# Performance work log

Hardware: AMD Instinct MI355X
Metric: run time of the kernel (lower is better)

The kernel has to match this reference:

```python
import jax, jax.numpy as jnp
import numpy as np
import math

B, NQ, HID = 1, 512, 4096
H, KVH, D = 32, 8, 128
NPRE, TOPK = 4096, 64
NREP = H // KVH


def _rope_tables(nq, d, base=10000.0):
    inv_freq = 1.0 / (base ** (np.arange(0, d, 2, dtype=np.float32) / d))
    freqs = np.outer(np.arange(nq, dtype=np.float32), inv_freq)  # [nq, d/2]
    emb = np.concatenate([freqs, freqs], axis=-1)                # [nq, d]
    return jnp.asarray(np.cos(emb))[None], jnp.asarray(np.sin(emb))[None]


def setup_inputs() -> dict:
    key = jax.random.key(0)
    ks = jax.random.split(key, 8)
    cos, sin = _rope_tables(NQ, D)
    wscale = 0.02
    return {
        "hidden_states": jax.random.normal(ks[0], (B, NQ, HID), jnp.float32),
        "cos": cos.astype(jnp.float32),
        "sin": sin.astype(jnp.float32),
        "prefix_key": jax.random.normal(ks[1], (B, KVH, NPRE, D), jnp.float32),
        "prefix_value": jax.random.normal(ks[2], (B, KVH, NPRE, D), jnp.float32),
        "Wq": jax.random.normal(ks[3], (HID, H * D), jnp.float32) * wscale,
        "Wk": jax.random.normal(ks[4], (HID, KVH * D), jnp.float32) * wscale,
        "Wv": jax.random.normal(ks[5], (HID, KVH * D), jnp.float32) * wscale,
        "Wo": jax.random.normal(ks[6], (H * D, HID), jnp.float32) * wscale,
    }


def _rotate_half(x):
    x1, x2 = jnp.split(x, 2, axis=-1)
    return jnp.concatenate([-x2, x1], axis=-1)


def _apply_rope(x, cos, sin):
    # x: [B, h, N, D]; cos/sin: [B, N, D] -> unsqueeze head dim (HF convention)
    c, s = cos[:, None], sin[:, None]
    return x * c + _rotate_half(x) * s


def _repeat_kv(x, n_rep):
    # [B, kvH, N, D] -> [B, kvH*n_rep, N, D] (repeat_interleave on head dim)
    b, kvh, n, d = x.shape
    return jnp.broadcast_to(x[:, :, None], (b, kvh, n_rep, n, d)).reshape(b, kvh * n_rep, n, d)


def reference(hidden_states, cos, sin, prefix_key, prefix_value, Wq, Wk, Wv, Wo):
    inv_sqrt_d = 1.0 / math.sqrt(D)

    q = (hidden_states @ Wq).reshape(B, NQ, H, D).transpose(0, 2, 1, 3)    # [B,H,Nq,D]
    k = (hidden_states @ Wk).reshape(B, NQ, KVH, D).transpose(0, 2, 1, 3)  # [B,kvH,Nq,D]
    v = (hidden_states @ Wv).reshape(B, NQ, KVH, D).transpose(0, 2, 1, 3)

    q = _apply_rope(q, cos, sin)
    k = _apply_rope(k, cos, sin)

    sk = _repeat_kv(k, NREP).reshape(B * H, NQ, D)            # suffix keys
    sv = _repeat_kv(v, NREP).reshape(B * H, NQ, D)            # suffix values
    pk = _repeat_kv(prefix_key, NREP).reshape(B * H, NPRE, D)  # FAISS DB keys (exact IP index)
    pv = _repeat_kv(prefix_value, NREP).reshape(B * H, NPRE, D)
    qf = q.reshape(B * H, NQ, D)

    # --- exact top-k inner-product search over prefix (== FAISS IndexFlatIP), scaled by 1/sqrt(D)
    prefix_scores = jnp.einsum('bnd,bmd->bnm', qf, pk) * inv_sqrt_d        # [BH,Nq,Npre]
    topk_values, topk_indices = jax.lax.top_k(prefix_scores, TOPK)         # [BH,Nq,k]

    topk_exp = jnp.exp(topk_values)
    topk_exp_sums = topk_exp.sum(axis=-1)                                  # [BH,Nq]

    # --- dense causal suffix attention (unnormalized, exp without max-shift, as in source)
    score_dense = jnp.einsum('bnd,bmd->bnm', qf, sk) * inv_sqrt_d          # [BH,Nq,Nq]
    causal = jnp.tril(jnp.ones((NQ, NQ), bool))
    score_dense = jnp.where(causal[None], score_dense, -jnp.inf)
    dense_exp = jnp.exp(score_dense)
    dense_exp_sums = dense_exp.sum(axis=-1)                                # [BH,Nq]

    denom = (topk_exp_sums + dense_exp_sums)[..., None]                    # shared softmax denom
    attn_topk = topk_exp / denom                                           # [BH,Nq,k]
    attn_dense = dense_exp / denom                                         # [BH,Nq,Nq]

    # --- sparse (COO) matmul with prefix values == gather + weighted sum
    bh_idx = jnp.arange(B * H)[:, None, None]
    gathered_pv = pv[bh_idx, topk_indices]                                 # [BH,Nq,k,D]
    xhat = jnp.einsum('bnk,bnkd->bnd', attn_topk, gathered_pv)
    xhat = xhat + attn_dense @ sv                                          # [BH,Nq,D]

    out = xhat.reshape(B, H, NQ, D).transpose(0, 2, 1, 3).reshape(B, NQ, H * D)
    return out @ Wo                                                        # [B,Nq,HID]
```

## Files before the change

kernel.cpp:

```cpp
#include <hip/hip_runtime.h>

#define DEV static __device__ __forceinline__

typedef _Float16 f16;
typedef __attribute__((ext_vector_type(8))) _Float16 f16x8;
typedef __attribute__((ext_vector_type(4))) _Float16 f16x4;
typedef __attribute__((ext_vector_type(4))) float    f32x4;

#define SCALE_QK 0.08838834764831845f

DEV float u2f(unsigned x){ union{unsigned u; float f;} c; c.u = x; return c.f; }

DEV void gload16(const f16* g, f16* l){
  __builtin_amdgcn_global_load_lds((const __attribute__((address_space(1))) void*)g,
                                   (__attribute__((address_space(3))) void*)l, 16, 0, 0);
}

template<int BM, int BN>
DEV void gemm_core3(const f16* At, int lda, const f16* Bt, int ldb, int K,
                    f32x4 (&acc)[BM/32][BN/32], f16* As, f16* Bs){
  constexpr int MR = BM / 32, NR = BN / 32;
  constexpr int ABUF = BM * 64, BBUF = BN * 64;
  static_assert(BM == 64 && BN == 64, "4 loads/wave/stage assumed");
  const int tid  = threadIdx.x;
  const int lane = tid & 63, w = tid >> 6;
  const int wr = w >> 1, wc = w & 1;
  const int lr = lane & 15, hi8 = (lane >> 4) * 8;
  const int srow = lane >> 3;
  const int sg   = (lane & 7) ^ srow;

  auto stage = [&](int buf, int k0){
#pragma unroll
    for (int i = 0; i < 2; ++i){
      const int ga = w + i * 4;
      gload16(At + (size_t)(ga * 8 + srow) * lda + k0 + sg * 8, As + buf * ABUF + ga * 512);
    }
#pragma unroll
    for (int i = 0; i < 2; ++i){
      const int gb = w + i * 4;
      gload16(Bt + (size_t)(gb * 8 + srow) * ldb + k0 + sg * 8, Bs + buf * BBUF + gb * 512);
    }
  };

  const int nt = K / 64;
  stage(0, 0);
  if (nt > 1) stage(1, 64);
  for (int t = 0; t < nt; ++t){
    if (t + 1 < nt) asm volatile("s_waitcnt vmcnt(4)" ::: "memory");
    else            asm volatile("s_waitcnt vmcnt(0)" ::: "memory");
    __builtin_amdgcn_sched_barrier(0);
    __builtin_amdgcn_s_barrier();
    __builtin_amdgcn_sched_barrier(0);
    const f16* Ab = As + (t % 3) * ABUF;
    const f16* Bb = Bs + (t % 3) * BBUF;
#pragma unroll
    for (int kk = 0; kk < 64; kk += 32){
      f16x8 a[MR], b[NR];
#pragma unroll
      for (int mi = 0; mi < MR; ++mi){
        const int row = wr * (BM / 2) + mi * 16 + lr;
        const int col = ((((kk + hi8) >> 3) ^ (row & 7)) << 3);
        a[mi] = *reinterpret_cast<const f16x8*>(&Ab[row * 64 + col]);
      }
#pragma unroll
      for (int ni = 0; ni < NR; ++ni){
        const int row = wc * (BN / 2) + ni * 16 + lr;
        const int col = ((((kk + hi8) >> 3) ^ (row & 7)) << 3);
        b[ni] = *reinterpret_cast<const f16x8*>(&Bb[row * 64 + col]);
      }
#pragma unroll
      for (int mi = 0; mi < MR; ++mi)
#pragma unroll
        for (int ni = 0; ni < NR; ++ni)
          acc[mi][ni] = __builtin_amdgcn_mfma_f32_16x16x32_f16(a[mi], b[ni], acc[mi][ni], 0, 0, 0);
    }
    if (t + 2 < nt) stage((t + 2) % 3, (t + 2) * 64);
  }
}

__global__ __launch_bounds__(256) void kcast(const float* __restrict__ in,
                                             f16* __restrict__ out, int n){
  int i = (blockIdx.x * 256 + threadIdx.x) * 4;
  if (i < n){
    f32x4 x = *reinterpret_cast<const f32x4*>(in + i);
    f16x4 y = { (f16)x[0], (f16)x[1], (f16)x[2], (f16)x[3] };
    *reinterpret_cast<f16x4*>(out + i) = y;
  }
}

__global__ __launch_bounds__(256) void ksplit(const float* __restrict__ in,
                                              f16* __restrict__ hi,
                                              f16* __restrict__ lo, int n4){
  int i = blockIdx.x * 256 + threadIdx.x;
  if (i < n4){
    f32x4 x = reinterpret_cast<const f32x4*>(in)[i];
    f16x4 h, l;
#pragma unroll
    for (int j = 0; j < 4; ++j){
      h[j] = (f16)x[j];
      l[j] = (f16)(x[j] - (float)h[j]);
    }
    reinterpret_cast<f16x4*>(hi)[i] = h;
    reinterpret_cast<f16x4*>(lo)[i] = l;
  }
}

__global__ __launch_bounds__(256) void ktransw(const float* __restrict__ in,
                                               f16* __restrict__ out, int R, int C){
  __shared__ float t[64][65];
  const int c0 = blockIdx.x * 64, r0 = blockIdx.y * 64;
  const int fx = threadIdx.x & 15;
  const int ry = threadIdx.x >> 4;
#pragma unroll
  for (int i = 0; i < 4; ++i){
    const int row = ry + i * 16;
    f32x4 v = *reinterpret_cast<const f32x4*>(&in[(size_t)(r0 + row) * C + c0 + fx * 4]);
    t[row][fx * 4 + 0] = v[0];
    t[row][fx * 4 + 1] = v[1];
    t[row][fx * 4 + 2] = v[2];
    t[row][fx * 4 + 3] = v[3];
  }
  __syncthreads();
  const int rx = threadIdx.x & 15;
  const int cy = threadIdx.x >> 4;
#pragma unroll
  for (int i = 0; i < 4; ++i){
    const int cc = cy + i * 16;
    f16x4 v = { (f16)t[4 * rx + 0][cc], (f16)t[4 * rx + 1][cc],
                (f16)t[4 * rx + 2][cc], (f16)t[4 * rx + 3][cc] };
    *reinterpret_cast<f16x4*>(&out[(size_t)(c0 + cc) * R + r0 + rx * 4]) = v;
  }
}

__global__ __launch_bounds__(256) void ktrans3w(const float* __restrict__ Wq,
                                                const float* __restrict__ Wk,
                                                const float* __restrict__ Wv,
                                                f16* __restrict__ wqkvT){
  __shared__ float t[64][65];
  const int bx = blockIdx.x;
  const float* in; f16* out; int C, cx;
  if (bx < 64)      { in = Wq; out = wqkvT;                        C = 4096; cx = bx; }
  else if (bx < 80) { in = Wk; out = wqkvT + (size_t)4096 * 4096;  C = 1024; cx = bx - 64; }
  else              { in = Wv; out = wqkvT + (size_t)5120 * 4096;  C = 1024; cx = bx - 80; }
  const int c0 = cx * 64, r0 = blockIdx.y * 64;
  const int fx = threadIdx.x & 15;
  const int ry = threadIdx.x >> 4;
#pragma unroll
  for (int i = 0; i < 4; ++i){
    const int row = ry + i * 16;
    f32x4 v = *reinterpret_cast<const f32x4*>(&in[(size_t)(r0 + row) * C + c0 + fx * 4]);
    t[row][fx * 4 + 0] = v[0];
    t[row][fx * 4 + 1] = v[1];
    t[row][fx * 4 + 2] = v[2];
    t[row][fx * 4 + 3] = v[3];
  }
  __syncthreads();
  const int rx = threadIdx.x & 15;
  const int cy = threadIdx.x >> 4;
#pragma unroll
  for (int i = 0; i < 4; ++i){
    const int cc = cy + i * 16;
    f16x4 v = { (f16)t[4 * rx + 0][cc], (f16)t[4 * rx + 1][cc],
                (f16)t[4 * rx + 2][cc], (f16)t[4 * rx + 3][cc] };
    *reinterpret_cast<f16x4*>(&out[(size_t)(c0 + cc) * 4096 + r0 + rx * 4]) = v;
  }
}

__global__ __launch_bounds__(256) void kgemm_qkv(const f16* __restrict__ A,
                                                 const f16* __restrict__ B,
                                                 float* __restrict__ qf,
                                                 float* __restrict__ kf,
                                                 f16* __restrict__ vbuf){
  __shared__ __align__(16) f16 As[3 * 64 * 64];
  __shared__ __align__(16) f16 Bs[3 * 64 * 64];
  const int orig = blockIdx.x + (blockIdx.y << 3);
  const int xcd = orig & 7, idx = orig >> 3;
  const int n_t = xcd * 12 + idx % 12;
  const int m_t = idx / 12;
  const int m0 = m_t * 64, n0 = n_t * 64;
  f32x4 acc[2][2];
#pragma unroll
  for (int i = 0; i < 2; ++i)
#pragma unroll
    for (int j = 0; j < 2; ++j){ f32x4 z = {0.f,0.f,0.f,0.f}; acc[i][j] = z; }
  gemm_core3<64,64>(A + (size_t)m0 * 4096, 4096, B + (size_t)n0 * 4096, 4096, 4096, acc, As, Bs);
  const int tid = threadIdx.x, lane = tid & 63, w = tid >> 6;
  const int wr = w >> 1, wc = w & 1, lr = lane & 15, hg = lane >> 4;
#pragma unroll
  for (int mi = 0; mi < 2; ++mi)
#pragma unroll
    for (int ni = 0; ni < 2; ++ni)
#pragma unroll
      for (int j = 0; j < 4; ++j){
        int rown = m0 + wr * 32 + mi * 16 + hg * 4 + j;
        int col  = n0 + wc * 32 + ni * 16 + lr;
        float vv = acc[mi][ni][j];
        if (col < 4096){
          int hh = col >> 7, dd = col & 127;
          qf[((size_t)hh * 512 + rown) * 128 + dd] = vv;
        } else if (col < 5120){
          int c2 = col - 4096; int hh = c2 >> 7, dd = c2 & 127;
          kf[((size_t)hh * 512 + rown) * 128 + dd] = vv;
        } else {
          int c2 = col - 5120; int hh = c2 >> 7, dd = c2 & 127;
          vbuf[((size_t)hh * 512 + rown) * 128 + dd] = (f16)vv;
        }
      }
}

__global__ __launch_bounds__(256) void krope_split(const float* __restrict__ qf,
                                                   const float* __restrict__ kf,
                                                   const float* __restrict__ cosb,
                                                   const float* __restrict__ sinb,
                                                   f16* __restrict__ qh, f16* __restrict__ ql,
                                                   f16* __restrict__ kh, f16* __restrict__ kl){
  int e = blockIdx.x * 256 + threadIdx.x;
  const int QP = 32 * 512 * 64;
  const float* src; f16 *oh, *ol; int e2;
  if (e < QP){ src = qf; oh = qh; ol = ql; e2 = e; }
  else       { src = kf; oh = kh; ol = kl; e2 = e - QP; }
  int rem = e2 & 32767, n = rem >> 6, d = rem & 63;
  size_t base = ((size_t)(e2 >> 15) * 512 + n) * 128;
  float x0 = src[base + d], x1 = src[base + d + 64];
  float c = cosb[n * 128 + d], s = sinb[n * 128 + d];
  float y0 = x0 * c - x1 * s;
  float y1 = x1 * c + x0 * s;
  f16 h0 = (f16)y0; oh[base + d]      = h0; ol[base + d]      = (f16)(y0 - (float)h0);
  f16 h1 = (f16)y1; oh[base + d + 64] = h1; ol[base + d + 64] = (f16)(y1 - (float)h1);
}

__global__ __launch_bounds__(512) void kgemm_score3(const f16* __restrict__ qh,
                                                    const f16* __restrict__ ql,
                                                    const f16* __restrict__ pkh,
                                                    const f16* __restrict__ pkl,
                                                    float* __restrict__ pscoreG,
                                                    int h0){
  __shared__ __align__(16) f16 Ah[128 * 64];
  __shared__ __align__(16) f16 Al[128 * 64];
  __shared__ __align__(16) f16 Bh[2 * 128 * 64];
  __shared__ __align__(16) f16 Bl[2 * 128 * 64];
  const int hl = blockIdx.z, h = h0 + hl, kvh = h >> 2;
  const int m0 = blockIdx.x * 128, n0 = blockIdx.y * 256;
  const f16* qhp = qh + ((size_t)h * 512 + m0) * 128;
  const f16* qlp = ql + ((size_t)h * 512 + m0) * 128;
  const f16* bhp = pkh + ((size_t)kvh * 4096 + n0) * 128;
  const f16* blp = pkl + ((size_t)kvh * 4096 + n0) * 128;
  f32x4 acc[4][4];
#pragma unroll
  for (int i = 0; i < 4; ++i)
#pragma unroll
    for (int j = 0; j < 4; ++j){ f32x4 z = {0.f,0.f,0.f,0.f}; acc[i][j] = z; }

  const int tid  = threadIdx.x;
  const int lane = tid & 63, w = tid >> 6;
  const int wr = w >> 2, wc = w & 3;
  const int lr = lane & 15, hi8 = (lane >> 4) * 8;
  const int srow = lane >> 3;
  const int sg   = (lane & 7) ^ srow;

  for (int k0 = 0; k0 < 128; k0 += 64){
    __syncthreads();
    for (int i = w; i < 16; i += 8){
      const int row = i * 8 + srow;
      const size_t go = (size_t)row * 128 + k0 + sg * 8;
      gload16(qhp + go, Ah + i * 512);
      gload16(qlp + go, Al + i * 512);
    }
    for (int i = w; i < 32; i += 8){
      const int row = i * 8 + srow;
      const size_t go = (size_t)row * 128 + k0 + sg * 8;
      gload16(bhp + go, Bh + i * 512);
      gload16(blp + go, Bl + i * 512);
    }
    __syncthreads();
#pragma unroll
    for (int kk = 0; kk < 64; kk += 32){
      f16x8 ah[4], al[4];
#pragma unroll
      for (int mi = 0; mi < 4; ++mi){
        const int row = wr * 64 + mi * 16 + lr;
        const int col = ((((kk + hi8) >> 3) ^ (row & 7)) << 3);
        ah[mi] = *reinterpret_cast<const f16x8*>(&Ah[row * 64 + col]);
        al[mi] = *reinterpret_cast<const f16x8*>(&Al[row * 64 + col]);
      }
#pragma unroll
      for (int ni = 0; ni < 4; ++ni){
        const int rowb = wc * 64 + ni * 16 + lr;
        const int colb = ((((kk + hi8) >> 3) ^ (rowb & 7)) << 3);
        f16x8 bh = *reinterpret_cast<const f16x8*>(&Bh[rowb * 64 + colb]);
        f16x8 bl = *reinterpret_cast<const f16x8*>(&Bl[rowb * 64 + colb]);
#pragma unroll
        for (int mi = 0; mi < 4; ++mi){
          acc[mi][ni] = __builtin_amdgcn_mfma_f32_16x16x32_f16(ah[mi], bh, acc[mi][ni], 0, 0, 0);
          acc[mi][ni] = __builtin_amdgcn_mfma_f32_16x16x32_f16(ah[mi], bl, acc[mi][ni], 0, 0, 0);
          acc[mi][ni] = __builtin_amdgcn_mfma_f32_16x16x32_f16(al[mi], bh, acc[mi][ni], 0, 0, 0);
        }
      }
    }
  }
  const int hg = lane >> 4;
#pragma unroll
  for (int mi = 0; mi < 4; ++mi)
#pragma unroll
    for (int ni = 0; ni < 4; ++ni)
#pragma unroll
      for (int j = 0; j < 4; ++j){
        int rown = m0 + wr * 64 + mi * 16 + hg * 4 + j;
        int col  = n0 + wc * 64 + ni * 16 + lr;
        pscoreG[((size_t)hl * 512 + rown) * 4096 + col] = acc[mi][ni][j] * SCALE_QK;
      }
}

__global__ __launch_bounds__(256) void ktopk(const unsigned* __restrict__ pscoreG,
                                             const float* __restrict__ pvf,
                                             float* __restrict__ xt,
                                             float* __restrict__ tsum,
                                             int h0){
  const int b = blockIdx.x;
  const int h = h0 + (b >> 9), kvh = h >> 2;
  const size_t hn = (size_t)h * 512 + (b & 511);
  __shared__ unsigned hist[256];
  __shared__ unsigned wtot[4];
  __shared__ unsigned wmax[4];
  __shared__ unsigned wtg[4], wte[4];
  __shared__ float    wred[4];
  __shared__ int   sidx[64];
  __shared__ float sw[64];
  __shared__ float red[256];
  __shared__ unsigned scal[2];
  const int tid = threadIdx.x, lane = tid & 63, wv = tid >> 6;
  const unsigned* rowp = pscoreG + ((size_t)b << 12) + tid * 16;
  unsigned key[16];
#pragma unroll
  for (int i = 0; i < 4; ++i)
    *reinterpret_cast<uint4*>(&key[i * 4]) = *reinterpret_cast<const uint4*>(&rowp[i * 4]);
#pragma unroll
  for (int k = 0; k < 16; ++k)
    key[k] = (key[k] & 0x80000000u) ? ~key[k] : (key[k] | 0x80000000u);

  unsigned pref, need;
  {
    unsigned mb = 0;
#pragma unroll
    for (int k = 0; k < 16; ++k) mb = max(mb, key[k] >> 24);
#pragma unroll
    for (int s2 = 32; s2 > 0; s2 >>= 1) mb = max(mb, (unsigned)__shfl_xor((int)mb, s2, 64));
    if (lane == 0) wmax[wv] = mb;
    __syncthreads();
    mb = max(max(wmax[0], wmax[1]), max(wmax[2], wmax[3]));
    __syncthreads();
    unsigned cum = 0, cur = mb;
    for (;;){
      unsigned cnt = 0, nxt = 0;
#pragma unroll
      for (int k = 0; k < 16; ++k){
        unsigned byte_ = key[k] >> 24;
        cnt += (byte_ == cur);
        if (byte_ < cur) nxt = max(nxt, byte_);
      }
#pragma unroll
      for (int s2 = 32; s2 > 0; s2 >>= 1){
        cnt += (unsigned)__shfl_xor((int)cnt, s2, 64);
        nxt  = max(nxt, (unsigned)__shfl_xor((int)nxt, s2, 64));
      }
      if (lane == 0){ wtot[wv] = cnt; wmax[wv] = nxt; }
      __syncthreads();
      unsigned tc = wtot[0] + wtot[1] + wtot[2] + wtot[3];
      unsigned tn = max(max(wmax[0], wmax[1]), max(wmax[2], wmax[3]));
      if (cum + tc >= 64u){ pref = cur; need = 64u - cum; break; }
      cum += tc; cur = tn;
      __syncthreads();
    }
    __syncthreads();
  }

#pragma unroll
  for (int lvl = 1; lvl < 3; ++lvl){
    const int sh = 24 - lvl * 8;
    hist[tid] = 0; __syncthreads();
#pragma unroll
    for (int k = 0; k < 16; ++k){
      if ((key[k] >> (sh + 8)) == pref) atomicAdd(&hist[(key[k] >> sh) & 255u], 1u);
    }
    __syncthreads();
    unsigned hval = hist[tid];
    unsigned sfx = hval;
#pragma unroll
    for (int s2 = 1; s2 < 64; s2 <<= 1){
      unsigned o = __shfl_down(sfx, s2, 64);
      if (lane + s2 < 64) sfx += o;
    }
    if (lane == 0) wtot[wv] = sfx;
    __syncthreads();
    unsigned add = 0;
#pragma unroll
    for (int w2 = 0; w2 < 4; ++w2) if (w2 > wv) add += wtot[w2];
    unsigned inc = sfx + add;
    unsigned abv = inc - hval;
    if (inc >= need && abv < need){ scal[0] = (unsigned)tid; scal[1] = need - abv; }
    __syncthreads();
    pref = (pref << 8) | scal[0];
    need = scal[1];
    __syncthreads();
  }
  const unsigned P = pref;

  int cgt = 0, ceq = 0;
#pragma unroll
  for (int k = 0; k < 16; ++k){
    unsigned t24 = key[k] >> 8;
    if (t24 > P) ++cgt; else if (t24 == P) ++ceq;
  }
  unsigned pg = (unsigned)cgt, pe = (unsigned)ceq;
#pragma unroll
  for (int s2 = 1; s2 < 64; s2 <<= 1){
    unsigned og_ = __shfl_up(pg, s2, 64);
    unsigned oe_ = __shfl_up(pe, s2, 64);
    if (lane >= s2){ pg += og_; pe += oe_; }
  }
  if (lane == 63){ wtg[wv] = pg; wte[wv] = pe; }
  __syncthreads();
  unsigned addg = 0, adde = 0, totg = 0;
#pragma unroll
  for (int w2 = 0; w2 < 4; ++w2){
    totg += wtg[w2];
    if (w2 < wv){ addg += wtg[w2]; adde += wte[w2]; }
  }
  const int totgt = (int)totg;
  const int slots = 64 - totgt;
  int og = (int)(pg + addg) - cgt;
  int oe = (int)(pe + adde) - ceq;
  float wsum = 0.f;
#pragma unroll
  for (int k = 0; k < 16; ++k){
    unsigned t24 = key[k] >> 8;
    unsigned orig = (key[k] & 0x80000000u) ? (key[k] & 0x7FFFFFFFu) : ~key[k];
    if (t24 > P){
      float e = __expf(u2f(orig));
      sidx[og] = tid * 16 + k; sw[og] = e; wsum += e; ++og;
    } else if (t24 == P){
      if (oe < slots){
        float e = __expf(u2f(orig));
        sidx[totgt + oe] = tid * 16 + k; sw[totgt + oe] = e; wsum += e;
      }
      ++oe;
    }
  }
#pragma unroll
  for (int s2 = 32; s2 > 0; s2 >>= 1) wsum += __shfl_xor(wsum, s2, 64);
  if (lane == 0) wred[wv] = wsum;
  __syncthreads();
  if (tid == 0) tsum[hn] = wred[0] + wred[1] + wred[2] + wred[3];

  const int d = tid & 127, half = tid >> 7;
  float acc = 0.f;
  const float* pvb = pvf + (size_t)kvh * 4096 * 128;
  for (int i = half * 32; i < half * 32 + 32; ++i)
    acc += sw[i] * pvb[(size_t)sidx[i] * 128 + d];
  red[tid] = acc;
  __syncthreads();
  if (tid < 128) xt[hn * 128 + tid] = red[tid] + red[tid + 128];
}

__global__ __launch_bounds__(256) void kdense(const f16* __restrict__ qh,
                                              const f16* __restrict__ ql,
                                              const f16* __restrict__ kh,
                                              const f16* __restrict__ kl,
                                              const f16* __restrict__ v16,
                                              float* __restrict__ dsum,
                                              float* __restrict__ xd){
  const int ntile = blockIdx.x, h = blockIdx.y, kvh = h >> 2;
  const int n0 = ntile * 64;
  __shared__ __align__(16) f16 Ksh[64 * 136];
  __shared__ __align__(16) f16 Ksl[64 * 136];
  __shared__ __align__(16) f16 VT[128 * 72];
  __shared__ __align__(16) f16 Ps[64 * 72];
  const int tid = threadIdx.x, lane = tid & 63, w = tid >> 6;
  const int lr = lane & 15, hg = lane >> 4, hi8 = hg * 8;

  f16x8 aqh[4], aql[4];
  {
    const size_t qoff = ((size_t)h * 512 + n0 + w * 16 + lr) * 128;
#pragma unroll
    for (int c = 0; c < 4; ++c){
      aqh[c] = *reinterpret_cast<const f16x8*>(&qh[qoff + c * 32 + hi8]);
      aql[c] = *reinterpret_cast<const f16x8*>(&ql[qoff + c * 32 + hi8]);
    }
  }
  f32x4 o[8];
#pragma unroll
  for (int i = 0; i < 8; ++i){ f32x4 z = {0.f,0.f,0.f,0.f}; o[i] = z; }
  float dp[4] = {0.f, 0.f, 0.f, 0.f};

  for (int mt = 0; mt <= ntile; ++mt){
    const int m0 = mt * 64;
#pragma unroll
    for (int i = 0; i < 4; ++i){
      int vv = tid + i * 256; int row = vv >> 4, kc = (vv & 15) * 8;
      const size_t ko = ((size_t)kvh * 512 + m0 + row) * 128 + kc;
      *reinterpret_cast<f16x8*>(&Ksh[row * 136 + kc]) = *reinterpret_cast<const f16x8*>(&kh[ko]);
      *reinterpret_cast<f16x8*>(&Ksl[row * 136 + kc]) = *reinterpret_cast<const f16x8*>(&kl[ko]);
    }
#pragma unroll
    for (int i = 0; i < 8; ++i){
      int vv = tid + i * 256; int m = vv >> 5, d4 = (vv & 31) * 4;
      f16x4 x = *reinterpret_cast<const f16x4*>(&v16[((size_t)kvh * 512 + m0 + m) * 128 + d4]);
      VT[(d4 + 0) * 72 + m] = x[0];
      VT[(d4 + 1) * 72 + m] = x[1];
      VT[(d4 + 2) * 72 + m] = x[2];
      VT[(d4 + 3) * 72 + m] = x[3];
    }
    __syncthreads();
    f32x4 s[4];
#pragma unroll
    for (int j = 0; j < 4; ++j){ f32x4 z = {0.f,0.f,0.f,0.f}; s[j] = z; }
#pragma unroll
    for (int c = 0; c < 4; ++c){
#pragma unroll
      for (int j = 0; j < 4; ++j){
        f16x8 bkh = *reinterpret_cast<const f16x8*>(&Ksh[(j * 16 + lr) * 136 + c * 32 + hi8]);
        f16x8 bkl = *reinterpret_cast<const f16x8*>(&Ksl[(j * 16 + lr) * 136 + c * 32 + hi8]);
        s[j] = __builtin_amdgcn_mfma_f32_16x16x32_f16(aqh[c], bkh, s[j], 0, 0, 0);
        s[j] = __builtin_amdgcn_mfma_f32_16x16x32_f16(aqh[c], bkl, s[j], 0, 0, 0);
        s[j] = __builtin_amdgcn_mfma_f32_16x16x32_f16(aql[c], bkh, s[j], 0, 0, 0);
      }
    }
#pragma unroll
    for (int j = 0; j < 4; ++j)
#pragma unroll
      for (int r = 0; r < 4; ++r){
        int ng = n0 + w * 16 + hg * 4 + r;
        int mg = m0 + j * 16 + lr;
        float p = (mg <= ng) ? __expf(s[j][r] * SCALE_QK) : 0.f;
        dp[r] += p;
        Ps[(w * 16 + hg * 4 + r) * 72 + j * 16 + lr] = (f16)p;
      }
    __syncthreads();
#pragma unroll
    for (int kk = 0; kk < 64; kk += 32){
      f16x8 pa = *reinterpret_cast<const f16x8*>(&Ps[(w * 16 + lr) * 72 + kk + hi8]);
#pragma unroll
      for (int dt = 0; dt < 8; ++dt){
        f16x8 bv = *reinterpret_cast<const f16x8*>(&VT[(dt * 16 + lr) * 72 + kk + hi8]);
        o[dt] = __builtin_amdgcn_mfma_f32_16x16x32_f16(pa, bv, o[dt], 0, 0, 0);
      }
    }
    __syncthreads();
  }
#pragma unroll
  for (int r = 0; r < 4; ++r){
    float vs = dp[r];
#pragma unroll
    for (int off2 = 1; off2 < 16; off2 <<= 1) vs += __shfl_xor(vs, off2, 64);
    if (lr == 0) dsum[h * 512 + n0 + w * 16 + hg * 4 + r] = vs;
  }
#pragma unroll
  for (int dt = 0; dt < 8; ++dt)
#pragma unroll
    for (int r = 0; r < 4; ++r){
      int ng = n0 + w * 16 + hg * 4 + r;
      xd[((size_t)h * 512 + ng) * 128 + dt * 16 + lr] = o[dt][r];
    }
}

__global__ __launch_bounds__(256) void kcombine(const float* __restrict__ xt,
                                                const float* __restrict__ xd,
                                                const float* __restrict__ tsum,
                                                const float* __restrict__ dsum,
                                                f16* __restrict__ xh16){
  int e = blockIdx.x * 256 + threadIdx.x;
  int hn = e >> 7, d = e & 127;
  int h = hn >> 9, n = hn & 511;
  float denom = tsum[hn] + dsum[hn];
  float v = (xt[e] + xd[e]) / denom;
  xh16[(size_t)n * 4096 + h * 128 + d] = (f16)v;
}

__global__ __launch_bounds__(256) void kgemm_out(const f16* __restrict__ A,
                                                 const f16* __restrict__ B,
                                                 float* __restrict__ out){
  __shared__ __align__(16) f16 As[3 * 64 * 64];
  __shared__ __align__(16) f16 Bs[3 * 64 * 64];
  const int orig = blockIdx.x + (blockIdx.y << 3);
  const int xcd = orig & 7, idx = orig >> 3;
  const int n_t = xcd * 8 + idx % 8;
  const int m_t = idx / 8;
  const int m0 = m_t * 64, n0 = n_t * 64;
  f32x4 acc[2][2];
#pragma unroll
  for (int i = 0; i < 2; ++i)
#pragma unroll
    for (int j = 0; j < 2; ++j){ f32x4 z = {0.f,0.f,0.f,0.f}; acc[i][j] = z; }
  gemm_core3<64,64>(A + (size_t)m0 * 4096, 4096, B + (size_t)n0 * 4096, 4096, 4096, acc, As, Bs);
  const int tid = threadIdx.x, lane = tid & 63, w = tid >> 6;
  const int wr = w >> 1, wc = w & 1, lr = lane & 15, hg = lane >> 4;
#pragma unroll
  for (int mi = 0; mi < 2; ++mi)
#pragma unroll
    for (int ni = 0; ni < 2; ++ni)
#pragma unroll
      for (int j = 0; j < 4; ++j){
        int rown = m0 + wr * 32 + mi * 16 + hg * 4 + j;
        int col  = n0 + wc * 32 + ni * 16 + lr;
        out[(size_t)rown * 4096 + col] = acc[mi][ni][j];
      }
}

extern "C" void kernel_launch(void* const* d_in, const int* in_sizes, int n_in,
                              void* d_out, int out_size, void* d_ws, size_t ws_size,
                              hipStream_t stream){
  (void)in_sizes; (void)n_in; (void)out_size;
  const float* hs   = (const float*)d_in[0];
  const float* cosb = (const float*)d_in[1];
  const float* sinb = (const float*)d_in[2];
  const float* pk   = (const float*)d_in[3];
  const float* pv   = (const float*)d_in[4];
  const float* Wq   = (const float*)d_in[5];
  const float* Wk   = (const float*)d_in[6];
  const float* Wv   = (const float*)d_in[7];
  const float* Wo   = (const float*)d_in[8];
  float* out = (float*)d_out;

  char* ws = (char*)d_ws;
  size_t off = 0;
  auto alloc = [&](size_t bytes) -> void* {
    void* p = ws + off; off += (bytes + 255) & ~(size_t)255; return p;
  };
  f16*  h16    = (f16*)alloc((size_t)512 * 4096 * 2);
  f16*  wqkvT  = (f16*)alloc((size_t)6144 * 4096 * 2);
  f16*  pkh    = (f16*)alloc((size_t)8 * 4096 * 128 * 2);
  f16*  pkl    = (f16*)alloc((size_t)8 * 4096 * 128 * 2);
  f16*  v16    = (f16*)alloc((size_t)8 * 512 * 128 * 2);
  f16*  qhh    = (f16*)alloc((size_t)32 * 512 * 128 * 2);
  f16*  qll    = (f16*)alloc((size_t)32 * 512 * 128 * 2);
  f16*  khh    = (f16*)alloc((size_t)8 * 512 * 128 * 2);
  f16*  kll    = (f16*)alloc((size_t)8 * 512 * 128 * 2);
  float* xd    = (float*)alloc((size_t)32 * 512 * 128 * 4);
  float* qf32  = (float*)alloc((size_t)32 * 512 * 128 * 4);
  float* kf32  = (float*)alloc((size_t)8 * 512 * 128 * 4);

  f16*   woT     = wqkvT;
  float* xt      = qf32;
  float* tsum    = kf32;
  float* dsum    = kf32 + 32 * 512;
  f16*   xh16    = h16;

  const size_t bigBytes = (size_t)8 * 512 * 4096 * 4;
  const bool   big      = (ws_size >= off + bigBytes + 256);
  float* pscoreUse = big ? (float*)(ws + off) : (float*)wqkvT;
  const int hN = big ? 8 : 4;

  kcast<<<2048, 256, 0, stream>>>(hs, h16, 512 * 4096);
  ksplit<<<4096, 256, 0, stream>>>(pk, pkh, pkl, 8 * 4096 * 128 / 4);
  ktrans3w<<<dim3(96, 64), 256, 0, stream>>>(Wq, Wk, Wv, wqkvT);

  kgemm_qkv<<<dim3(8, 96), 256, 0, stream>>>(h16, wqkvT, qf32, kf32, v16);
  krope_split<<<5120, 256, 0, stream>>>(qf32, kf32, cosb, sinb, qhh, qll, khh, kll);

  for (int h0 = 0; h0 < 32; h0 += hN){
    kgemm_score3<<<dim3(4, 16, hN), 512, 0, stream>>>(qhh, qll, pkh, pkl, pscoreUse, h0);
    ktopk<<<hN * 512, 256, 0, stream>>>((const unsigned*)pscoreUse, pv, xt, tsum, h0);
  }

  ktransw<<<dim3(64, 64), 256, 0, stream>>>(Wo, woT, 4096, 4096);

  kdense<<<dim3(8, 32), 256, 0, stream>>>(qhh, qll, khh, kll, v16, dsum, xd);
  kcombine<<<8192, 256, 0, stream>>>(xt, xd, tsum, dsum, xh16);
  kgemm_out<<<dim3(8, 64), 256, 0, stream>>>(xh16, woT, out);
}
```

Baseline: 375.0 us.

## Run top-k selection with one wavefront per row, removing block barriers

The top-k kernel now assigns each 4096-score row to a single 64-lane wavefront (64 keys per lane) instead of a 256-thread block, with four rows per block. All __syncthreads-based cross-wave reductions in the radix select, prefix scans and gather are replaced by wave shuffles, ballots and per-wave LDS slices. The goal is to remove barrier and cross-wave reduction overhead in the selection loop. In exchange each lane holds 64 keys in registers, which raises VGPR pressure and may lower occupancy, and the per-row gather has less parallelism.

Result: slower. 428.5 us (+14.3%).

```diff
diff --git a/kernel.cpp b/kernel.cpp
--- a/kernel.cpp
+++ b/kernel.cpp
@@ -316,150 +316,141 @@
                                              float* __restrict__ xt,
                                              float* __restrict__ tsum,
                                              int h0){
-  const int b = blockIdx.x;
-  const int h = h0 + (b >> 9), kvh = h >> 2;
-  const size_t hn = (size_t)h * 512 + (b & 511);
-  __shared__ unsigned hist[256];
-  __shared__ unsigned wtot[4];
-  __shared__ unsigned wmax[4];
-  __shared__ unsigned wtg[4], wte[4];
-  __shared__ float    wred[4];
-  __shared__ int   sidx[64];
-  __shared__ float sw[64];
-  __shared__ float red[256];
-  __shared__ unsigned scal[2];
-  const int tid = threadIdx.x, lane = tid & 63, wv = tid >> 6;
-  const unsigned* rowp = pscoreG + ((size_t)b << 12) + tid * 16;
-  unsigned key[16];
-#pragma unroll
-  for (int i = 0; i < 4; ++i)
+  __shared__ unsigned shist[4][256];
+  __shared__ int   ssidx[4][64];
+  __shared__ float ssw[4][64];
+  const int lane = threadIdx.x & 63, wv = threadIdx.x >> 6;
+  const int r = blockIdx.x * 4 + wv;
+  const int h = h0 + (r >> 9), kvh = h >> 2;
+  const size_t hn = (size_t)h * 512 + (r & 511);
+  const unsigned* rowp = pscoreG + ((size_t)r << 12) + lane * 64;
+
+  unsigned key[64];
+#pragma unroll
+  for (int i = 0; i < 16; ++i)
     *reinterpret_cast<uint4*>(&key[i * 4]) = *reinterpret_cast<const uint4*>(&rowp[i * 4]);
 #pragma unroll
-  for (int k = 0; k < 16; ++k)
+  for (int k = 0; k < 64; ++k)
     key[k] = (key[k] & 0x80000000u) ? ~key[k] : (key[k] | 0x80000000u);
 
   unsigned pref, need;
   {
     unsigned mb = 0;
 #pragma unroll
-    for (int k = 0; k < 16; ++k) mb = max(mb, key[k] >> 24);
-#pragma unroll
-    for (int s2 = 32; s2 > 0; s2 >>= 1) mb = max(mb, (unsigned)__shfl_xor((int)mb, s2, 64));
-    if (lane == 0) wmax[wv] = mb;
-    __syncthreads();
-    mb = max(max(wmax[0], wmax[1]), max(wmax[2], wmax[3]));
-    __syncthreads();
+    for (int k = 0; k < 64; ++k) mb = max(mb, key[k] >> 24);
+#pragma unroll
+    for (int s = 32; s > 0; s >>= 1) mb = max(mb, (unsigned)__shfl_xor((int)mb, s, 64));
     unsigned cum = 0, cur = mb;
     for (;;){
       unsigned cnt = 0, nxt = 0;
 #pragma unroll
-      for (int k = 0; k < 16; ++k){
-        unsigned byte_ = key[k] >> 24;
-        cnt += (byte_ == cur);
-        if (byte_ < cur) nxt = max(nxt, byte_);
-      }
-#pragma unroll
-      for (int s2 = 32; s2 > 0; s2 >>= 1){
-        cnt += (unsigned)__shfl_xor((int)cnt, s2, 64);
-        nxt  = max(nxt, (unsigned)__shfl_xor((int)nxt, s2, 64));
-      }
-      if (lane == 0){ wtot[wv] = cnt; wmax[wv] = nxt; }
-      __syncthreads();
-      unsigned tc = wtot[0] + wtot[1] + wtot[2] + wtot[3];
-      unsigned tn = max(max(wmax[0], wmax[1]), max(wmax[2], wmax[3]));
-      if (cum + tc >= 64u){ pref = cur; need = 64u - cum; break; }
-      cum += tc; cur = tn;
-      __syncthreads();
-    }
-    __syncthreads();
+      for (int k = 0; k < 64; ++k){
+        unsigned by = key[k] >> 24;
+        cnt += (by == cur);
+        if (by < cur) nxt = max(nxt, by);
+      }
+#pragma unroll
+      for (int s = 32; s > 0; s >>= 1){
+        cnt += (unsigned)__shfl_xor((int)cnt, s, 64);
+        nxt  = max(nxt, (unsigned)__shfl_xor((int)nxt, s, 64));
+      }
+      if (cum + cnt >= 64u){ pref = cur; need = 64u - cum; break; }
+      cum += cnt; cur = nxt;
+    }
   }
 
 #pragma unroll
   for (int lvl = 1; lvl < 3; ++lvl){
     const int sh = 24 - lvl * 8;
-    hist[tid] = 0; __syncthreads();
-#pragma unroll
-    for (int k = 0; k < 16; ++k){
-      if ((key[k] >> (sh + 8)) == pref) atomicAdd(&hist[(key[k] >> sh) & 255u], 1u);
-    }
-    __syncthreads();
-    unsigned hval = hist[tid];
-    unsigned sfx = hval;
-#pragma unroll
-    for (int s2 = 1; s2 < 64; s2 <<= 1){
-      unsigned o = __shfl_down(sfx, s2, 64);
-      if (lane + s2 < 64) sfx += o;
-    }
-    if (lane == 0) wtot[wv] = sfx;
-    __syncthreads();
-    unsigned add = 0;
-#pragma unroll
-    for (int w2 = 0; w2 < 4; ++w2) if (w2 > wv) add += wtot[w2];
-    unsigned inc = sfx + add;
-    unsigned abv = inc - hval;
-    if (inc >= need && abv < need){ scal[0] = (unsigned)tid; scal[1] = need - abv; }
-    __syncthreads();
-    pref = (pref << 8) | scal[0];
-    need = scal[1];
-    __syncthreads();
+#pragma unroll
+    for (int j = 0; j < 4; ++j) shist[wv][lane * 4 + j] = 0;
+    asm volatile("s_waitcnt lgkmcnt(0)" ::: "memory");
+    __builtin_amdgcn_sched_barrier(0);
+#pragma unroll
+    for (int k = 0; k < 64; ++k)
+      if ((key[k] >> (sh + 8)) == pref)
+        atomicAdd(&shist[wv][(key[k] >> sh) & 255u], 1u);
+    asm volatile("s_waitcnt lgkmcnt(0)" ::: "memory");
+    __builtin_amdgcn_sched_barrier(0);
+    unsigned hb[4];
+#pragma unroll
+    for (int j = 0; j < 4; ++j) hb[j] = shist[wv][lane * 4 + j];
+    unsigned local = hb[0] + hb[1] + hb[2] + hb[3];
+    unsigned sfx = local;
+#pragma unroll
+    for (int s = 1; s < 64; s <<= 1){
+      unsigned o = __shfl_down(sfx, s, 64);
+      if (lane + s < 64) sfx += o;
+    }
+    unsigned run = sfx - local;
+    unsigned mySel = 0, myNeed = 0; bool found = false;
+#pragma unroll
+    for (int j = 3; j >= 0; --j){
+      unsigned inc = run + hb[j];
+      if (!found && inc >= need && run < need){
+        mySel = (unsigned)(lane * 4 + j); myNeed = need - run; found = true;
+      }
+      run = inc;
+    }
+    unsigned long long mk = __ballot(found);
+    int src = __ffsll((unsigned long long)mk) - 1;
+    pref = (pref << 8) | (unsigned)__shfl((int)mySel, src, 64);
+    need = (unsigned)__shfl((int)myNeed, src, 64);
   }
   const unsigned P = pref;
 
   int cgt = 0, ceq = 0;
 #pragma unroll
-  for (int k = 0; k < 16; ++k){
-    unsigned t24 = key[k] >> 8;
-    if (t24 > P) ++cgt; else if (t24 == P) ++ceq;
-  }
-  unsigned pg = (unsigned)cgt, pe = (unsigned)ceq;
-#pragma unroll
-  for (int s2 = 1; s2 < 64; s2 <<= 1){
-    unsigned og_ = __shfl_up(pg, s2, 64);
-    unsigned oe_ = __shfl_up(pe, s2, 64);
-    if (lane >= s2){ pg += og_; pe += oe_; }
-  }
-  if (lane == 63){ wtg[wv] = pg; wte[wv] = pe; }
-  __syncthreads();
-  unsigned addg = 0, adde = 0, totg = 0;
-#pragma unroll
-  for (int w2 = 0; w2 < 4; ++w2){
-    totg += wtg[w2];
-    if (w2 < wv){ addg += wtg[w2]; adde += wte[w2]; }
-  }
-  const int totgt = (int)totg;
+  for (int k = 0; k < 64; ++k){
+    unsigned t = key[k] >> 8;
+    cgt += (t > P); ceq += (t == P);
+  }
+  int pg = cgt, pe = ceq;
+#pragma unroll
+  for (int s = 1; s < 64; s <<= 1){
+    int og_ = __shfl_up(pg, s, 64);
+    int oe_ = __shfl_up(pe, s, 64);
+    if (lane >= s){ pg += og_; pe += oe_; }
+  }
+  const int totgt = __shfl(pg, 63, 64);
   const int slots = 64 - totgt;
-  int og = (int)(pg + addg) - cgt;
-  int oe = (int)(pe + adde) - ceq;
+  int og = pg - cgt, oe = pe - ceq;
   float wsum = 0.f;
 #pragma unroll
-  for (int k = 0; k < 16; ++k){
-    unsigned t24 = key[k] >> 8;
-    unsigned orig = (key[k] & 0x80000000u) ? (key[k] & 0x7FFFFFFFu) : ~key[k];
-    if (t24 > P){
+  for (int k = 0; k < 64; ++k){
+    unsigned t = key[k] >> 8;
+    if (t > P){
+      unsigned orig = (key[k] & 0x80000000u) ? (key[k] & 0x7FFFFFFFu) : ~key[k];
       float e = __expf(u2f(orig));
-      sidx[og] = tid * 16 + k; sw[og] = e; wsum += e; ++og;
-    } else if (t24 == P){
+      ssidx[wv][og] = lane * 64 + k; ssw[wv][og] = e; wsum += e; ++og;
+    } else if (t == P){
       if (oe < slots){
+        unsigned orig = (key[k] & 0x80000000u) ? (key[k] & 0x7FFFFFFFu) : ~key[k];
         float e = __expf(u2f(orig));
-        sidx[totgt + oe] = tid * 16 + k; sw[totgt + oe] = e; wsum += e;
+        ssidx[wv][totgt + oe] = lane * 64 + k; ssw[wv][totgt + oe] = e; wsum += e;
       }
       ++oe;
     }
   }
 #pragma unroll
-  for (int s2 = 32; s2 > 0; s2 >>= 1) wsum += __shfl_xor(wsum, s2, 64);
-  if (lane == 0) wred[wv] = wsum;
-  __syncthreads();
-  if (tid == 0) tsum[hn] = wred[0] + wred[1] + wred[2] + wred[3];
-
-  const int d = tid & 127, half = tid >> 7;
-  float acc = 0.f;
+  for (int s = 32; s > 0; s >>= 1) wsum += __shfl_xor(wsum, s, 64);
+  if (lane == 0) tsum[hn] = wsum;
+  asm volatile("s_waitcnt lgkmcnt(0)" ::: "memory");
+  __builtin_amdgcn_sched_barrier(0);
+
   const float* pvb = pvf + (size_t)kvh * 4096 * 128;
-  for (int i = half * 32; i < half * 32 + 32; ++i)
-    acc += sw[i] * pvb[(size_t)sidx[i] * 128 + d];
-  red[tid] = acc;
-  __syncthreads();
-  if (tid < 128) xt[hn * 128 + tid] = red[tid] + red[tid + 128];
+  float a0 = 0.f, a1 = 0.f, b0 = 0.f, b1 = 0.f;
+#pragma unroll 4
+  for (int i = 0; i < 64; i += 2){
+    float w0 = ssw[wv][i];     int i0 = ssidx[wv][i];
+    float w1 = ssw[wv][i + 1]; int i1 = ssidx[wv][i + 1];
+    a0 += w0 * pvb[(size_t)i0 * 128 + lane];
+    b0 += w0 * pvb[(size_t)i0 * 128 + 64 + lane];
+    a1 += w1 * pvb[(size_t)i1 * 128 + lane];
+    b1 += w1 * pvb[(size_t)i1 * 128 + 64 + lane];
+  }
+  xt[hn * 128 + lane]      = a0 + a1;
+  xt[hn * 128 + 64 + lane] = b0 + b1;
 }
 
 __global__ __launch_bounds__(256) void kdense(const f16* __restrict__ qh,
@@ -659,7 +650,7 @@
 
   for (int h0 = 0; h0 < 32; h0 += hN){
     kgemm_score3<<<dim3(4, 16, hN), 512, 0, stream>>>(qhh, qll, pkh, pkl, pscoreUse, h0);
-    ktopk<<<hN * 512, 256, 0, stream>>>((const unsigned*)pscoreUse, pv, xt, tsum, h0);
+    ktopk<<<hN * 128, 256, 0, stream>>>((const unsigned*)pscoreUse, pv, xt, tsum, h0);
   }
 
   ktransw<<<dim3(64, 64), 256, 0, stream>>>(Wo, woT, 4096, 4096);
```
